# Kernel optimization log

Measured on AMD Instinct MI355X. Metric: run time of the kernel, lower is better.

## Reference

```python
import jax, jax.numpy as jnp
import numpy as np

VOCAB = 50000
D = 200          # word_dimension
A = 32           # aspect_dimension
NUM_NEG = 5
AVG_RATING = 3.5
LR_RATING = 1.0
LR_ABAE = 1.0
N = 4096         # reviews in batch
L = 128          # tokens per review
B = 1024         # users / items
H = 16           # avg history length (flat = B*H)


def setup_inputs() -> dict:
    key = jax.random.key(0)
    ks = jax.random.split(key, 12)
    hist = jax.random.randint(ks[0], (N, L), 0, VOCAB)
    rev_pos = jax.random.normal(ks[1], (N, D), jnp.float32)
    rev_neg = jax.random.normal(ks[2], (N * NUM_NEG, D), jnp.float32)
    user = jax.random.randint(ks[3], (B,), 0, B)
    item = jax.random.randint(ks[4], (B,), 0, B)
    label = jax.random.uniform(ks[5], (B,), jnp.float32) * 4.0 + 1.0
    user_hist_idx = jax.random.randint(ks[6], (B * H,), 0, N)
    item_hist_idx = jax.random.randint(ks[7], (B * H,), 0, N)
    # segment ids: each user/item owns H consecutive entries (ragged in general)
    user_seg_ids = jnp.repeat(jnp.arange(B), H)
    item_seg_ids = jnp.repeat(jnp.arange(B), H)
    word_emb = jax.random.normal(ks[8], (VOCAB, D), jnp.float32) * 0.1
    M_w = jax.random.normal(ks[9], (D, D), jnp.float32) * (1.0 / np.sqrt(D))
    W_w = jax.random.normal(ks[10], (A, D), jnp.float32) * (1.0 / np.sqrt(D))
    W_b = jnp.zeros((A,), jnp.float32)
    T_w = jax.random.normal(ks[11], (D, A), jnp.float32) * (1.0 / np.sqrt(A))
    return {
        'historical_review': hist, 'review_positive': rev_pos,
        'review_negative': rev_neg, 'user': user, 'item': item,
        'label': label, 'user_hist_idx': user_hist_idx,
        'user_seg_ids': user_seg_ids, 'item_hist_idx': item_hist_idx,
        'item_seg_ids': item_seg_ids, 'word_emb': word_emb,
        'M_w': M_w, 'W_w': W_w, 'W_b': W_b, 'T_w': T_w,
    }


def _l2norm(x, axis):
    # matches F.normalize(p=2, eps=1e-12)
    n = jnp.sqrt(jnp.sum(x * x, axis=axis, keepdims=True))
    return x / jnp.maximum(n, 1e-12)


def reference(historical_review, review_positive, review_negative, user, item,
              label, user_hist_idx, user_seg_ids, item_hist_idx, item_seg_ids,
              word_emb, M_w, W_w, W_b, T_w):
    n, l = historical_review.shape
    d = word_emb.shape[1]
    e_w = word_emb[historical_review]                       # [N,L,D]
    # dx = (e_w @ M^T) . y_s  -> attention logits over tokens
    dx = jnp.einsum('nld,nd->nl', e_w @ M_w.T, review_positive)
    ax = jax.nn.softmax(dx, axis=1)                          # [N,L]
    # NOTE: original uses .view(N, D, L) (a reshape, NOT a transpose) -- faithful
    z_s = jnp.einsum('ndl,nl->nd', e_w.reshape(n, d, l), ax)  # [N,D]
    p_t = jax.nn.softmax(z_s @ W_w.T + W_b, axis=1)          # [N,A]
    r_s = p_t @ T_w.T                                        # [N,D]

    c1 = jnp.sum(_l2norm(r_s, 1) * _l2norm(z_s, 1), axis=-1)  # [N]
    c1r = jnp.repeat(c1, NUM_NEG)                            # [N*NUM_NEG]
    z_n = review_negative.reshape(n, NUM_NEG, d)
    c2 = jnp.sum(_l2norm(z_n, 2) * _l2norm(r_s, 1)[:, None, :], axis=-1).reshape(-1)
    # MarginRankingLoss(margin=0, target=1): mean(max(0, c2 - c1))
    J_loss = jnp.mean(jnp.maximum(0.0, c2 - c1r))
    Tn = _l2norm(T_w, 0)                                     # normalize columns
    U_loss = jnp.mean((Tn.T @ Tn - jnp.eye(A, dtype=T_w.dtype)) ** 2)
    abae_loss = U_loss + J_loss

    nb = label.shape[0]
    def seg_mean(idx, seg):
        g = r_s[idx]                                         # ragged gather [F,D]
        s = jax.ops.segment_sum(g, seg, num_segments=nb)
        c = jax.ops.segment_sum(jnp.ones(idx.shape[0], r_s.dtype), seg, num_segments=nb)
        return s / c[:, None]

    u_emb = seg_mean(user_hist_idx, user_seg_ids)            # [B,D]
    i_emb = seg_mean(item_hist_idx, item_seg_ids)            # [B,D]
    prediction = jnp.sum(u_emb * i_emb, axis=-1) + AVG_RATING
    rating_loss = jnp.mean((prediction - label) ** 2)
    obj = LR_RATING * rating_loss + LR_ABAE * abae_loss
    return (obj, rating_loss, abae_loss)
```

## Files before the change

### kernel.cpp

```cpp
#include <hip/hip_runtime.h>

#define NN 4096
#define LL 128
#define DD 200
#define AA 32
#define NEG 5
#define BB 1024

#define WS_RS    0
#define WS_ACC   (NN*DD)

template<int C, int RM>
__device__ __forceinline__ float dpp_add(float v){
  int t = __builtin_amdgcn_update_dpp(0, __float_as_int(v), C, RM, 0xf, false);
  return v + __int_as_float(t);
}
template<int C, int RM>
__device__ __forceinline__ float dpp_fmax(float v){
  int t = __builtin_amdgcn_update_dpp(__float_as_int(-3.0e38f), __float_as_int(v),
                                      C, RM, 0xf, false);
  return fmaxf(v, __int_as_float(t));
}
__device__ __forceinline__ float sum64(float v){
  v = dpp_add<0xB1, 0xF>(v);
  v = dpp_add<0x4E, 0xF>(v);
  v = dpp_add<0x124,0xF>(v);
  v = dpp_add<0x128,0xF>(v);
  v = dpp_add<0x142,0xA>(v);
  v = dpp_add<0x143,0xC>(v);
  return v;
}
__device__ __forceinline__ float max64(float v){
  v = dpp_fmax<0xB1, 0xF>(v);
  v = dpp_fmax<0x4E, 0xF>(v);
  v = dpp_fmax<0x124,0xF>(v);
  v = dpp_fmax<0x128,0xF>(v);
  v = dpp_fmax<0x142,0xA>(v);
  v = dpp_fmax<0x143,0xC>(v);
  return v;
}
__device__ __forceinline__ float sum8(float v){
  v = dpp_add<0xB1, 0xF>(v);
  v = dpp_add<0x4E, 0xF>(v);
  v = dpp_add<0x124,0xF>(v);
  return v;
}
__device__ __forceinline__ float rdlane(float v, int l){
  return __int_as_float(__builtin_amdgcn_readlane(__float_as_int(v), l));
}
__device__ __forceinline__ float dot4(float4 a, float4 b){
  return a.x*b.x + a.y*b.y + a.z*b.z + a.w*b.w;
}

__global__ __launch_bounds__(256, 7)
void k_main(const int* __restrict__ hist, const float* __restrict__ rev_pos,
            const float* __restrict__ rev_neg, const float* __restrict__ word_emb,
            const float* __restrict__ M_w, const float* __restrict__ W_w,
            const float* __restrict__ W_b, const float* __restrict__ T_w,
            float* __restrict__ rs_out, float* __restrict__ acc)
{
  __shared__ __align__(16) float smem[1704];
  float* y_l  = smem;
  float* dxax = smem + 208;
  float* zsm  = smem + 336;
  float* r_l  = smem + 536;
  float* lsps = smem + 736;
  float* sc   = smem + 768;
  int*   hrowl= (int*)(smem + 776);
  float* ypart= smem + 904;

  const int n = blockIdx.x;
  const int t = threadIdx.x;
  const int w = t >> 6, j = t & 63;
  const int wu = __builtin_amdgcn_readfirstlane(w);

  if (t < DD) r_l[t] = rev_pos[(size_t)n * DD + t];
  if (t < LL) hrowl[t] = hist[(size_t)n * LL + t];
  __syncthreads();

  if (j < 50){
    float ax = 0.f, ay = 0.f, az = 0.f, aw = 0.f;
    const float* Mb = M_w + (50 * wu) * DD + 4 * j;
    const float* rb = r_l + 50 * wu;
#pragma unroll 10
    for (int dk = 0; dk < 50; ++dk){
      float rv = rb[dk];
      float4 m4 = *(const float4*)(Mb + dk * DD);
      ax = fmaf(rv, m4.x, ax); ay = fmaf(rv, m4.y, ay);
      az = fmaf(rv, m4.z, az); aw = fmaf(rv, m4.w, aw);
    }
    float4 o; o.x = ax; o.y = ay; o.z = az; o.w = aw;
    *(float4*)(ypart + wu * 200 + 4 * j) = o;
  }
  __syncthreads();
  if (t < DD) y_l[t] = ypart[t] + ypart[200 + t] + ypart[400 + t] + ypart[600 + t];
  __syncthreads();

  {
    float4 y4 = make_float4(0.f, 0.f, 0.f, 0.f);
    int col = 0;
    if (j < 50){ y4 = *(const float4*)(y_l + 4 * j); col = 4 * j; }
    const int* hrow_g = hist + (size_t)n * LL + 32 * wu;
#pragma unroll
    for (int k8 = 0; k8 < 4; ++k8){
      int rows[8];
#pragma unroll
      for (int i = 0; i < 8; ++i) rows[i] = hrow_g[8 * k8 + i];
      float4 g[8];
#pragma unroll
      for (int i = 0; i < 8; ++i)
        g[i] = *(const float4*)(word_emb + (size_t)rows[i] * DD + col);
#pragma unroll
      for (int i = 0; i < 8; ++i){
        float v = sum64(dot4(g[i], y4));
        if (j == 63) dxax[32 * wu + 8 * k8 + i] = v;
      }
    }
  }
  __syncthreads();

  if (w == 0){
    float a0 = dxax[j], a1 = dxax[j + 64];
    float M = rdlane(max64(fmaxf(a0, a1)), 63);
    float e0 = __expf(a0 - M), e1 = __expf(a1 - M);
    float S = rdlane(sum64(e0 + e1), 63);
    float inv = 1.f / S;
    dxax[j] = e0 * inv; dxax[j + 64] = e1 * inv;
  }
  __syncthreads();

  {
    const int q = j & 7, oct = j >> 3;
    float4 ax0 = *(const float4*)(dxax +      4 * q);
    float4 ax1 = *(const float4*)(dxax + 32 + 4 * q);
    float4 ax2 = *(const float4*)(dxax + 64 + 4 * q);
    float4 ax3 = *(const float4*)(dxax + 96 + 4 * q);

#pragma unroll
    for (int bp = 0; bp < 3; ++bp){
      int offA = 16 * bp + oct, offB = offA + 8;
      int dA = 50 * wu + offA,  dB = 50 * wu + offB;
      unsigned a0f = (unsigned)dA * 128u + 4u * (unsigned)q;
      unsigned b0f = (unsigned)dB * 128u + 4u * (unsigned)q;
      float4 gA[4], gB[4];
#pragma unroll
      for (int i = 0; i < 4; ++i){
        unsigned fa = a0f + 32u * i;
        unsigned ra = fa / 200u;
        gA[i] = *(const float4*)(word_emb + (size_t)hrowl[ra] * DD + (fa - ra * 200u));
      }
#pragma unroll
      for (int i = 0; i < 4; ++i){
        unsigned fb = b0f + 32u * i;
        unsigned rb = fb / 200u;
        gB[i] = *(const float4*)(word_emb + (size_t)hrowl[rb] * DD + (fb - rb * 200u));
      }
      float pA = dot4(gA[0],ax0) + dot4(gA[1],ax1) + dot4(gA[2],ax2) + dot4(gA[3],ax3);
      float pB = dot4(gB[0],ax0) + dot4(gB[1],ax1) + dot4(gB[2],ax2) + dot4(gB[3],ax3);
      float vA = sum8(pA), vB = sum8(pB);
      if (q == 0){ zsm[dA] = vA; zsm[dB] = vB; }
    }
    {
      int off = 48 + oct;
      int offc = off < 50 ? off : 49;
      int d2 = 50 * wu + offc;
      unsigned f0 = (unsigned)d2 * 128u + 4u * (unsigned)q;
      float4 g[4];
#pragma unroll
      for (int i = 0; i < 4; ++i){
        unsigned f = f0 + 32u * i;
        unsigned r = f / 200u;
        g[i] = *(const float4*)(word_emb + (size_t)hrowl[r] * DD + (f - r * 200u));
      }
      float p = dot4(g[0],ax0) + dot4(g[1],ax1) + dot4(g[2],ax2) + dot4(g[3],ax3);
      float v = sum8(p);
      if (q == 0 && off < 50) zsm[d2] = v;
    }
  }
  __syncthreads();

#pragma unroll
  for (int aa = 0; aa < 8; ++aa){
    int a = wu * 8 + aa;
    const float* Wr = W_w + a * DD;
    float p = zsm[j] * Wr[j] + zsm[j + 64] * Wr[j + 64] + zsm[j + 128] * Wr[j + 128];
    if (j < 8) p += zsm[j + 192] * Wr[j + 192];
    float v = sum64(p);
    if (j == 63) lsps[a] = v + W_b[a];
  }
  __syncthreads();

  if (w == 0){
    float v = (j < 32) ? lsps[j] : -3.0e38f;
    float M = rdlane(max64(v), 63);
    float e = __expf(v - M);
    float S = rdlane(sum64(e), 63);
    if (j < 32) lsps[j] = e / S;
  }
  __syncthreads();

  if (t < DD){
    const float4* Tq = (const float4*)(T_w + t * AA);
    float a = 0.f;
#pragma unroll
    for (int q = 0; q < 8; ++q){
      float4 tv = Tq[q];
      a += lsps[4*q]*tv.x + lsps[4*q+1]*tv.y + lsps[4*q+2]*tv.z + lsps[4*q+3]*tv.w;
    }
    r_l[t] = a;
    rs_out[(size_t)n * DD + t] = a;
  }
  __syncthreads();

  if (w == 0){
    float rr = 0, zz = 0, rz = 0;
    if (j < 50){
      float4 rv = *(float4*)(r_l + 4 * j);
      float4 zv = *(float4*)(zsm + 4 * j);
      rr = dot4(rv, rv); zz = dot4(zv, zv); rz = dot4(rv, zv);
    }
    rr = rdlane(sum64(rr), 63); zz = rdlane(sum64(zz), 63); rz = rdlane(sum64(rz), 63);
    if (j == 0){
      float nr = fmaxf(sqrtf(rr), 1e-12f);
      float nz = fmaxf(sqrtf(zz), 1e-12f);
      sc[0] = rz / (nr * nz);
      sc[1] = nr;
    }
  }
  __syncthreads();

  for (int g5 = w; g5 < NEG; g5 += 4){
    const float* neg = rev_neg + ((size_t)n * NEG + g5) * DD;
    float nn = 0, dr = 0;
    if (j < 50){
      float4 v = *(const float4*)(neg + 4 * j);
      float4 rv = *(float4*)(r_l + 4 * j);
      nn = dot4(v, v); dr = dot4(v, rv);
    }
    nn = rdlane(sum64(nn), 63); dr = rdlane(sum64(dr), 63);
    if (j == 0){
      float c2 = dr / (fmaxf(sqrtf(nn), 1e-12f) * sc[1]);
      sc[2 + g5] = fmaxf(0.f, c2 - sc[0]);
    }
  }
  __syncthreads();
  if (t == 0) atomicAdd(&acc[0], sc[2] + sc[3] + sc[4] + sc[5] + sc[6]);
}

__device__ __forceinline__ void finalize(float* acc, float* out){
  float R = atomicAdd(&acc[2], 0.f) / (float)BB;
  float J = atomicAdd(&acc[0], 0.f) / (float)(NN * NEG);
  float U = atomicAdd(&acc[1], 0.f);
  out[0] = R + U + J;
  out[1] = R;
  out[2] = U + J;
}

__global__ __launch_bounds__(256)
void k_tail(const int* __restrict__ u_idx, const int* __restrict__ i_idx,
            const float* __restrict__ rs, const float* __restrict__ label,
            const float* __restrict__ T_w, float* __restrict__ acc,
            float* __restrict__ out){
  __shared__ __align__(16) float smem[6500];
  const int b = blockIdx.x, t = threadIdx.x, w = t >> 6, j = t & 63;

  if (b == BB){
    float* Tl  = smem;
    float* nrm = smem + 6464;
    float* wred= smem + 6496;
    for (int i = t; i < DD * AA; i += 256){
      int d = i >> 5, a = i & 31;
      Tl[a * 202 + d] = T_w[i];
    }
    __syncthreads();
    if (t < AA){
      float s = 0.f;
      for (int d = 0; d < DD; d += 2){
        float2 v = *(float2*)&Tl[t * 202 + d];
        s += v.x * v.x + v.y * v.y;
      }
      nrm[t] = fmaxf(sqrtf(s), 1e-12f);
    }
    __syncthreads();
    int a = t >> 3, b0 = (t & 7) * 4;
    float d0 = 0, d1 = 0, d2 = 0, d3 = 0;
    for (int d = 0; d < DD; d += 2){
      float2 va = *(float2*)&Tl[a * 202 + d];
      float2 v0 = *(float2*)&Tl[(b0    ) * 202 + d];
      float2 v1 = *(float2*)&Tl[(b0 + 1) * 202 + d];
      float2 v2 = *(float2*)&Tl[(b0 + 2) * 202 + d];
      float2 v3 = *(float2*)&Tl[(b0 + 3) * 202 + d];
      d0 += va.x * v0.x + va.y * v0.y;
      d1 += va.x * v1.x + va.y * v1.y;
      d2 += va.x * v2.x + va.y * v2.y;
      d3 += va.x * v3.x + va.y * v3.y;
    }
    float na = nrm[a], gg = 0.f, g;
    g = d0 / (na * nrm[b0    ]) - (a == b0     ? 1.f : 0.f); gg += g * g;
    g = d1 / (na * nrm[b0 + 1]) - (a == b0 + 1 ? 1.f : 0.f); gg += g * g;
    g = d2 / (na * nrm[b0 + 2]) - (a == b0 + 2 ? 1.f : 0.f); gg += g * g;
    g = d3 / (na * nrm[b0 + 3]) - (a == b0 + 3 ? 1.f : 0.f); gg += g * g;
    float v = sum64(gg);
    if (j == 63) wred[w] = v;
    __syncthreads();
    if (t == 0){
      atomicAdd(&acc[1], (wred[0] + wred[1] + wred[2] + wred[3]) / (float)(AA * AA));
      __threadfence();
      int prev = atomicAdd((int*)acc + 8, 1);
      if (prev == BB) finalize(acc, out);
    }
    return;
  }

  int*   idxs = (int*)smem;
  float* wred = smem + 32;
  if (t < 16) idxs[t] = u_idx[b * 16 + t];
  else if (t < 32) idxs[t] = i_idx[b * 16 + (t - 16)];
  __syncthreads();
  float su = 0.f, si = 0.f;
  if (t < DD){
#pragma unroll
    for (int k = 0; k < 16; ++k) su += rs[(size_t)idxs[k] * DD + t];
#pragma unroll
    for (int k = 0; k < 16; ++k) si += rs[(size_t)idxs[16 + k] * DD + t];
  }
  float v = sum64(su * si);
  if (j == 63) wred[w] = v;
  __syncthreads();
  if (t == 0){
    float dot = wred[0] + wred[1] + wred[2] + wred[3];
    float pred = dot * (1.f / 256.f) + 3.5f;
    float e = pred - label[b];
    atomicAdd(&acc[2], e * e);
    __threadfence();
    int prev = atomicAdd((int*)acc + 8, 1);
    if (prev == BB) finalize(acc, out);
  }
}

extern "C" void kernel_launch(void* const* d_in, const int* in_sizes, int n_in,
                              void* d_out, int out_size, void* d_ws, size_t ws_size,
                              hipStream_t stream){
  const int*   hist     = (const int*)  d_in[0];
  const float* rev_pos  = (const float*)d_in[1];
  const float* rev_neg  = (const float*)d_in[2];
  const float* label    = (const float*)d_in[5];
  const int*   u_idx    = (const int*)  d_in[6];
  const int*   i_idx    = (const int*)  d_in[8];
  const float* word_emb = (const float*)d_in[10];
  const float* M_w      = (const float*)d_in[11];
  const float* W_w      = (const float*)d_in[12];
  const float* W_b      = (const float*)d_in[13];
  const float* T_w      = (const float*)d_in[14];

  float* ws   = (float*)d_ws;
  float* rs   = ws + WS_RS;
  float* accp = ws + WS_ACC;

  hipMemsetAsync(accp, 0, 64, stream);
  k_main<<<NN, 256, 0, stream>>>(hist, rev_pos, rev_neg, word_emb, M_w,
                                 W_w, W_b, T_w, rs, accp);
  k_tail<<<BB + 1, 256, 0, stream>>>(u_idx, i_idx, rs, label, T_w, accp,
                                     (float*)d_out);
}
```

Measured before the change: 270.4 us.

## Prefetch word-embedding gathers across stages with double-buffered register pipelines

Issues the first dx word-embedding gathers before the M_w·r matvec and its barriers, so their latency overlaps that compute. The remaining gathers are double-buffered so each chunk's loads are in flight while the previous chunk is reduced. The z-stage gathers are likewise started before the softmax barrier and pipelined in pairs. Launch bounds drop from 7 to 5 waves to make room for the extra live registers, which lowers occupancy.

```diff
diff --git a/kernel.cpp b/kernel.cpp
--- a/kernel.cpp
+++ b/kernel.cpp
@@ -52,7 +52,21 @@
   return a.x*b.x + a.y*b.y + a.z*b.z + a.w*b.w;
 }
 
-__global__ __launch_bounds__(256, 7)
+__device__ __forceinline__ void z_load(float4* buf, const float* __restrict__ we,
+                                       const int* hrowl, int d2, int q){
+  unsigned f0 = (unsigned)d2 * 128u + 4u * (unsigned)q;
+#pragma unroll
+  for (int i = 0; i < 4; ++i){
+    unsigned f = f0 + 32u * i;
+    unsigned r = f / 200u;
+    buf[i] = *(const float4*)(we + (size_t)hrowl[r] * DD + (f - r * 200u));
+  }
+}
+__device__ __forceinline__ float z_red(const float4* buf, const float4* ax){
+  return dot4(buf[0],ax[0]) + dot4(buf[1],ax[1]) + dot4(buf[2],ax[2]) + dot4(buf[3],ax[3]);
+}
+
+__global__ __launch_bounds__(256, 5)
 void k_main(const int* __restrict__ hist, const float* __restrict__ rev_pos,
             const float* __restrict__ rev_neg, const float* __restrict__ word_emb,
             const float* __restrict__ M_w, const float* __restrict__ W_w,
@@ -76,6 +90,22 @@
 
   if (t < DD) r_l[t] = rev_pos[(size_t)n * DD + t];
   if (t < LL) hrowl[t] = hist[(size_t)n * LL + t];
+
+  const int* hrow_g = hist + (size_t)n * LL + 32 * wu;
+  const int col = (j < 50) ? 4 * j : 0;
+  int rA[8], rB[8];
+  float4 gA[8], gB[8];
+#pragma unroll
+  for (int i = 0; i < 8; ++i) rA[i] = hrow_g[i];
+#pragma unroll
+  for (int i = 0; i < 8; ++i)
+    gA[i] = *(const float4*)(word_emb + (size_t)rA[i] * DD + col);
+#pragma unroll
+  for (int i = 0; i < 8; ++i) rB[i] = hrow_g[8 + i];
+#pragma unroll
+  for (int i = 0; i < 8; ++i)
+    gB[i] = *(const float4*)(word_emb + (size_t)rB[i] * DD + col);
+
   __syncthreads();
 
   if (j < 50){
@@ -98,25 +128,50 @@
 
   {
     float4 y4 = make_float4(0.f, 0.f, 0.f, 0.f);
-    int col = 0;
-    if (j < 50){ y4 = *(const float4*)(y_l + 4 * j); col = 4 * j; }
-    const int* hrow_g = hist + (size_t)n * LL + 32 * wu;
-#pragma unroll
-    for (int k8 = 0; k8 < 4; ++k8){
-      int rows[8];
-#pragma unroll
-      for (int i = 0; i < 8; ++i) rows[i] = hrow_g[8 * k8 + i];
-      float4 g[8];
-#pragma unroll
-      for (int i = 0; i < 8; ++i)
-        g[i] = *(const float4*)(word_emb + (size_t)rows[i] * DD + col);
-#pragma unroll
-      for (int i = 0; i < 8; ++i){
-        float v = sum64(dot4(g[i], y4));
-        if (j == 63) dxax[32 * wu + 8 * k8 + i] = v;
-      }
-    }
-  }
+    if (j < 50) y4 = *(const float4*)(y_l + 4 * j);
+#pragma unroll
+    for (int i = 0; i < 8; ++i){
+      float v = sum64(dot4(gA[i], y4));
+      if (j == 63) dxax[32 * wu + i] = v;
+    }
+#pragma unroll
+    for (int i = 0; i < 8; ++i) rA[i] = hrow_g[16 + i];
+#pragma unroll
+    for (int i = 0; i < 8; ++i)
+      gA[i] = *(const float4*)(word_emb + (size_t)rA[i] * DD + col);
+#pragma unroll
+    for (int i = 0; i < 8; ++i){
+      float v = sum64(dot4(gB[i], y4));
+      if (j == 63) dxax[32 * wu + 8 + i] = v;
+    }
+#pragma unroll
+    for (int i = 0; i < 8; ++i) rB[i] = hrow_g[24 + i];
+#pragma unroll
+    for (int i = 0; i < 8; ++i)
+      gB[i] = *(const float4*)(word_emb + (size_t)rB[i] * DD + col);
+#pragma unroll
+    for (int i = 0; i < 8; ++i){
+      float v = sum64(dot4(gA[i], y4));
+      if (j == 63) dxax[32 * wu + 16 + i] = v;
+    }
+#pragma unroll
+    for (int i = 0; i < 8; ++i){
+      float v = sum64(dot4(gB[i], y4));
+      if (j == 63) dxax[32 * wu + 24 + i] = v;
+    }
+  }
+
+  const int q = j & 7, oct = j >> 3;
+  int d2c[7];
+#pragma unroll
+  for (int k = 0; k < 7; ++k){
+    int off = 8 * k + oct;
+    d2c[k] = 50 * wu + (off < 50 ? off : 49);
+  }
+  float4 za[4], zb[4];
+  z_load(za, word_emb, hrowl, d2c[0], q);
+  z_load(zb, word_emb, hrowl, d2c[1], q);
+
   __syncthreads();
 
   if (w == 0){
@@ -130,52 +185,24 @@
   __syncthreads();
 
   {
-    const int q = j & 7, oct = j >> 3;
-    float4 ax0 = *(const float4*)(dxax +      4 * q);
-    float4 ax1 = *(const float4*)(dxax + 32 + 4 * q);
-    float4 ax2 = *(const float4*)(dxax + 64 + 4 * q);
-    float4 ax3 = *(const float4*)(dxax + 96 + 4 * q);
-
-#pragma unroll
-    for (int bp = 0; bp < 3; ++bp){
-      int offA = 16 * bp + oct, offB = offA + 8;
-      int dA = 50 * wu + offA,  dB = 50 * wu + offB;
-      unsigned a0f = (unsigned)dA * 128u + 4u * (unsigned)q;
-      unsigned b0f = (unsigned)dB * 128u + 4u * (unsigned)q;
-      float4 gA[4], gB[4];
-#pragma unroll
-      for (int i = 0; i < 4; ++i){
-        unsigned fa = a0f + 32u * i;
-        unsigned ra = fa / 200u;
-        gA[i] = *(const float4*)(word_emb + (size_t)hrowl[ra] * DD + (fa - ra * 200u));
-      }
-#pragma unroll
-      for (int i = 0; i < 4; ++i){
-        unsigned fb = b0f + 32u * i;
-        unsigned rb = fb / 200u;
-        gB[i] = *(const float4*)(word_emb + (size_t)hrowl[rb] * DD + (fb - rb * 200u));
-      }
-      float pA = dot4(gA[0],ax0) + dot4(gA[1],ax1) + dot4(gA[2],ax2) + dot4(gA[3],ax3);
-      float pB = dot4(gB[0],ax0) + dot4(gB[1],ax1) + dot4(gB[2],ax2) + dot4(gB[3],ax3);
-      float vA = sum8(pA), vB = sum8(pB);
-      if (q == 0){ zsm[dA] = vA; zsm[dB] = vB; }
-    }
-    {
-      int off = 48 + oct;
-      int offc = off < 50 ? off : 49;
-      int d2 = 50 * wu + offc;
-      unsigned f0 = (unsigned)d2 * 128u + 4u * (unsigned)q;
-      float4 g[4];
-#pragma unroll
-      for (int i = 0; i < 4; ++i){
-        unsigned f = f0 + 32u * i;
-        unsigned r = f / 200u;
-        g[i] = *(const float4*)(word_emb + (size_t)hrowl[r] * DD + (f - r * 200u));
-      }
-      float p = dot4(g[0],ax0) + dot4(g[1],ax1) + dot4(g[2],ax2) + dot4(g[3],ax3);
-      float v = sum8(p);
-      if (q == 0 && off < 50) zsm[d2] = v;
-    }
+    float4 axr[4];
+    axr[0] = *(const float4*)(dxax +      4 * q);
+    axr[1] = *(const float4*)(dxax + 32 + 4 * q);
+    axr[2] = *(const float4*)(dxax + 64 + 4 * q);
+    axr[3] = *(const float4*)(dxax + 96 + 4 * q);
+    float v;
+    v = sum8(z_red(za, axr)); if (q == 0) zsm[d2c[0]] = v;
+    z_load(za, word_emb, hrowl, d2c[2], q);
+    v = sum8(z_red(zb, axr)); if (q == 0) zsm[d2c[1]] = v;
+    z_load(zb, word_emb, hrowl, d2c[3], q);
+    v = sum8(z_red(za, axr)); if (q == 0) zsm[d2c[2]] = v;
+    z_load(za, word_emb, hrowl, d2c[4], q);
+    v = sum8(z_red(zb, axr)); if (q == 0) zsm[d2c[3]] = v;
+    z_load(zb, word_emb, hrowl, d2c[5], q);
+    v = sum8(z_red(za, axr)); if (q == 0) zsm[d2c[4]] = v;
+    z_load(za, word_emb, hrowl, d2c[6], q);
+    v = sum8(z_red(zb, axr)); if (q == 0) zsm[d2c[5]] = v;
+    v = sum8(z_red(za, axr)); if (q == 0 && oct < 2) zsm[d2c[6]] = v;
   }
   __syncthreads();
 
@@ -203,9 +230,9 @@
     const float4* Tq = (const float4*)(T_w + t * AA);
     float a = 0.f;
 #pragma unroll
-    for (int q = 0; q < 8; ++q){
-      float4 tv = Tq[q];
-      a += lsps[4*q]*tv.x + lsps[4*q+1]*tv.y + lsps[4*q+2]*tv.z + lsps[4*q+3]*tv.w;
+    for (int q8 = 0; q8 < 8; ++q8){
+      float4 tv = Tq[q8];
+      a += lsps[4*q8]*tv.x + lsps[4*q8+1]*tv.y + lsps[4*q8+2]*tv.z + lsps[4*q8+3]*tv.w;
     }
     r_l[t] = a;
     rs_out[(size_t)n * DD + t] = a;
```

New measurement: 318.8 us. +17.9%, slower.
